# Kernel tuning notes

Measured on AMD Instinct MI355X. Metric: run time of the kernel, lower is better.

Reference implementation:

```python
import jax, jax.numpy as jnp
import numpy as np

N_NODES = 50000
N_EDGES = 800000
N_GRAPHS = 500
NFEAT = 128
NHID = 64
NLAYER = 3
BN_EPS = 1e-5


def setup_inputs() -> dict:
    key = jax.random.key(0)
    ks = jax.random.split(key, 8)
    x = jax.random.normal(ks[0], (N_NODES, NFEAT), dtype=jnp.float32)
    edge_index = jax.random.randint(ks[1], (2, N_EDGES), 0, N_NODES)
    batch = jnp.sort(jax.random.randint(ks[2], (N_NODES,), 0, N_GRAPHS))
    Wt = jax.random.normal(ks[3], (NFEAT, NHID), dtype=jnp.float32) / np.float32(np.sqrt(NFEAT))
    bt = jnp.zeros((NHID,), jnp.float32)
    gamma0 = jnp.ones((NHID,), jnp.float32)
    beta0 = jnp.zeros((NHID,), jnp.float32)
    W1 = jax.random.normal(ks[4], (NLAYER, NHID, NHID), dtype=jnp.float32) / np.float32(np.sqrt(NHID))
    W2 = jax.random.normal(ks[5], (NLAYER, NHID, NHID), dtype=jnp.float32) / np.float32(np.sqrt(NHID))
    gammas = jnp.ones((NLAYER, NHID), jnp.float32)
    betas = jnp.zeros((NLAYER, NHID), jnp.float32)
    return dict(x=x, edge_index=edge_index, batch=batch, Wt=Wt, bt=bt,
                gamma0=gamma0, beta0=beta0, W1=W1, W2=W2, gammas=gammas, betas=betas)


def _bn(h, g, b):
    # BatchNorm1d training-mode math: batch mean, biased variance
    mean = jnp.mean(h, axis=0)
    var = jnp.mean((h - mean) ** 2, axis=0)
    return (h - mean) * jax.lax.rsqrt(var + BN_EPS) * g + b


def _pool_mean(h, batch):
    s = jax.ops.segment_sum(h, batch, num_segments=N_GRAPHS)
    cnt = jax.ops.segment_sum(jnp.ones((h.shape[0], 1), h.dtype), batch, num_segments=N_GRAPHS)
    return s / jnp.maximum(cnt, 1.0)


def _embed_std(h, batch):
    m = _pool_mean(h, batch)                      # [G, nhid]
    s = jnp.sqrt(_pool_mean((h - m[batch]) ** 2, batch))
    return m, s


def reference(x, edge_index, batch, Wt, bt, gamma0, beta0, W1, W2, gammas, betas):
    src, dst = edge_index[0], edge_index[1]
    h = _bn(x @ Wt + bt, gamma0, beta0)           # transform: Linear + BN
    e0, s0 = _embed_std(h, batch)

    def step(h, p):
        w1, w2, g, b = p
        agg = jax.ops.segment_sum(h[src], dst, num_segments=N_NODES)  # GIN sum-aggregation
        z = (h + agg)                              # (1+eps)*x + agg, eps=0
        z = jax.nn.relu(z @ w1) @ w2               # GINConv nn: Linear-ReLU-Linear (no bias)
        z = _bn(jax.nn.relu(z), g, b)              # act then BN
        e, s = _embed_std(z, batch)
        return z, (e, s)

    _, (es, ss) = jax.lax.scan(step, h, (W1, W2, gammas, betas))
    graph_embeds = jnp.concatenate([e0[None], es], axis=0)  # [nlayer+1, G, nhid]
    graph_stds = jnp.concatenate([s0[None], ss], axis=0)
    return graph_embeds, graph_stds
```

## Files before the change

kernel.cpp:

```cpp
#include <hip/hip_runtime.h>
#include <hip/hip_bf16.h>

#define NN 50000
#define NE 800000
#define NG 500
#define NF 128
#define NH 64
#define NB 256
#define NPB 196
#define EPB 4096
#define NBLK ((NE + EPB - 1)/EPB)
#define CSR_LDS 2048

typedef unsigned int u32;
typedef unsigned short u16;
typedef _Float16 h2 __attribute__((ext_vector_type(2)));
typedef _Float16 h8 __attribute__((ext_vector_type(8)));
typedef float f32x4 __attribute__((ext_vector_type(4)));

__device__ __forceinline__ float bf1(u16 v){ return __uint_as_float(((u32)v) << 16); }
__device__ __forceinline__ float h1(u16 v){ return (float)__builtin_bit_cast(_Float16, v); }
__device__ __forceinline__ u32 pk(float a, float b){
  return __builtin_bit_cast(u32, __builtin_amdgcn_cvt_pkrtz(a, b));
}
__device__ __forceinline__ h2 uph(u32 u){ return __builtin_bit_cast(h2, u); }
__device__ __forceinline__ u16 f16b(float f){ return __builtin_bit_cast(u16, (_Float16)f); }

__device__ __forceinline__ void cv8h(uint4 q, float* f){
  h2 v0 = uph(q.x), v1 = uph(q.y), v2 = uph(q.z), v3 = uph(q.w);
  f[0]=(float)v0.x; f[1]=(float)v0.y; f[2]=(float)v1.x; f[3]=(float)v1.y;
  f[4]=(float)v2.x; f[5]=(float)v2.y; f[6]=(float)v3.x; f[7]=(float)v3.y;
}

__device__ __forceinline__ h8 pack8(float4 p, float4 q){
  uint4 t;
  t.x = pk(p.x, p.y); t.y = pk(p.z, p.w);
  t.z = pk(q.x, q.y); t.w = pk(q.z, q.w);
  return __builtin_bit_cast(h8, t);
}
__device__ __forceinline__ f32x4 z4(){
  f32x4 v; v[0]=0.f; v[1]=0.f; v[2]=0.f; v[3]=0.f; return v;
}

__global__ __launch_bounds__(256) void k_init(const u32* __restrict__ xw, int* __restrict__ flag,
    const int* __restrict__ batch, int* __restrict__ starts,
    const float* __restrict__ Wt, const float* __restrict__ W1, const float* __restrict__ W2,
    u16* __restrict__ wtT, u16* __restrict__ w1T, u16* __restrict__ w2T){
  int b = blockIdx.x, tid = threadIdx.x;
  if (b < 48){
    int t = b*256 + tid;
    if (t < NH*NF){
      int c = t >> 7, k = t & 127;
      wtT[t] = f16b(Wt[(size_t)k*NH + c]);
    }
    if (t < 3*NH*NH){
      int l = t >> 12, c = (t >> 6) & 63, k = t & 63;
      w1T[t] = f16b(W1[(size_t)l*NH*NH + k*NH + c]);
      w2T[t] = f16b(W2[(size_t)l*NH*NH + k*NH + c]);
    }
  } else {
    if (tid < 64){
      u32 w = xw[tid];
      u32 lo = w & 0xFFFFu;
      u32 e = (lo >> 7) & 0xFFu;
      bool vote = (e >= 0x60u && e <= 0x8Fu);
      unsigned long long m = __ballot(vote);
      if (tid == 0) flag[0] = (__popcll(m) >= 32) ? 1 : 0;
    }
    for (int g = tid; g <= NG; g += 256){
      int lo = 0, hi = NN;
      while (lo < hi){ int mid = (lo + hi) >> 1; if (batch[mid] < g) lo = mid + 1; else hi = mid; }
      starts[g] = lo;
    }
  }
}


__global__ __launch_bounds__(256) void k_bhist(const int* __restrict__ ei, int* __restrict__ bcount,
    int* __restrict__ bstart, int* __restrict__ bcur, int* __restrict__ ticket){
  __shared__ int h[NB];
  __shared__ int part[NB];
  __shared__ int isLast;
  int tid = threadIdx.x;
  h[tid] = 0;
  __syncthreads();
  int e0 = blockIdx.x*EPB;
  #pragma unroll
  for (int i = 0; i < 16; i++){
    int e = e0 + i*256 + tid;
    if (e < NE) atomicAdd(&h[ei[NE + e] / NPB], 1);
  }
  __syncthreads();
  if (h[tid]) atomicAdd(&bcount[tid], h[tid]);
  __threadfence();
  if (tid == 0) isLast = (atomicAdd(ticket, 1) == (int)gridDim.x - 1);
  __syncthreads();
  if (!isLast) return;
  int v = atomicAdd(&bcount[tid], 0);
  part[tid] = v;
  __syncthreads();
  for (int off = 1; off < 256; off <<= 1){
    int u = (tid >= off) ? part[tid-off] : 0;
    __syncthreads();
    part[tid] += u;
    __syncthreads();
  }
  int ex = part[tid] - v;
  bstart[tid] = ex;
  bcur[tid] = ex;
  if (tid == 0) bstart[NB] = NE;
}

__global__ __launch_bounds__(256) void k_bscat(const int* __restrict__ ei,
    int* __restrict__ bcur, u32* __restrict__ pkE){
  __shared__ int h[NB];
  __shared__ int loff[NB];
  __shared__ int base[NB];
  __shared__ int part[NB];
  __shared__ u32 sv[EPB];
  int tid = threadIdx.x;
  h[tid] = 0;
  __syncthreads();
  int e0 = blockIdx.x*EPB;
  u32 meta[16], vals[16];
  #pragma unroll
  for (int i = 0; i < 16; i++){
    int e = e0 + i*256 + tid;
    if (e < NE){
      int s = ei[e], d = ei[NE + e];
      int b = d / NPB;
      int r = atomicAdd(&h[b], 1);
      meta[i] = ((u32)b << 16) | (u32)r;
      vals[i] = ((u32)d << 16) | (u32)s;
    } else meta[i] = 0xFFFFFFFFu;
  }
  __syncthreads();
  int cnt = h[tid];
  part[tid] = cnt;
  __syncthreads();
  for (int off = 1; off < 256; off <<= 1){
    int u = (tid >= off) ? part[tid-off] : 0;
    __syncthreads();
    part[tid] += u;
    __syncthreads();
  }
  loff[tid] = part[tid] - cnt;
  base[tid] = cnt ? atomicAdd(&bcur[tid], cnt) : 0;
  __syncthreads();
  #pragma unroll
  for (int i = 0; i < 16; i++){
    if (meta[i] != 0xFFFFFFFFu){
      int b = meta[i] >> 16, r = meta[i] & 0xFFFFu;
      sv[loff[b] + r] = vals[i];
    }
  }
  __syncthreads();
  int total = min(EPB, NE - e0);
  for (int j = tid; j < total; j += 256){
    u32 v = sv[j];
    int b = (int)(v >> 16) / NPB;
    pkE[base[b] + (j - loff[b])] = v;
  }
}

__global__ __launch_bounds__(256) void k_bfill(const u32* __restrict__ pkE,
    const int* __restrict__ bstart, int* __restrict__ rowptr, int* __restrict__ csr){
  __shared__ int part[NB];
  __shared__ int cur[NB];
  int b = blockIdx.x;
  int tid = threadIdx.x;
  int nb0 = b*NPB;
  int nr = min(NPB, NN - nb0);
  int rbeg = bstart[b], rend = bstart[b+1];
  part[tid] = 0;
  __syncthreads();
  for (int j = rbeg + tid; j < rend; j += 256){
    u32 pe = pkE[j];
    atomicAdd(&part[(int)(pe >> 16) - nb0], 1);
  }
  __syncthreads();
  int v = part[tid];
  __syncthreads();
  for (int off = 1; off < 256; off <<= 1){
    int u = (tid >= off) ? part[tid-off] : 0;
    __syncthreads();
    part[tid] += u;
    __syncthreads();
  }
  int ex = part[tid] - v;
  if (tid < nr) rowptr[nb0 + tid] = rbeg + ex;
  if (b == NB-1 && tid == 0) rowptr[NN] = NE;
  cur[tid] = ex;
  __syncthreads();
  for (int j = rbeg + tid; j < rend; j += 256){
    u32 pe = pkE[j];
    int node = (int)(pe >> 16) - nb0;
    int p = atomicAdd(&cur[node], 1);
    csr[rbeg + p] = (int)(pe & 0xFFFFu);
  }
}

__global__ __launch_bounds__(256) void k_transform_m(const float* __restrict__ x,
    const u16* __restrict__ wtT, const float* __restrict__ bt,
    u16* __restrict__ th, float* __restrict__ s1){
  __shared__ float sRed[8*NH];
  int tid = threadIdx.x;
  int w = tid >> 6, l = tid & 63;
  int lr = l & 15, kb = l >> 4;
  h8 bf[4][4];
  #pragma unroll
  for (int n = 0; n < 4; n++)
    #pragma unroll
    for (int kk = 0; kk < 4; kk++)
      bf[n][kk] = *(const h8*)&wtT[(size_t)(16*n + lr)*NF + kk*32 + kb*8];
  int node0 = blockIdx.x*64 + w*16;
  int rowA = node0 + lr; if (rowA > NN-1) rowA = NN-1;
  const float* xr = x + (size_t)rowA*NF + kb*8;
  f32x4 acc[4];
  #pragma unroll
  for (int n = 0; n < 4; n++) acc[n] = z4();
  #pragma unroll
  for (int kk = 0; kk < 4; kk++){
    float4 p = *(const float4*)(xr + kk*32);
    float4 q = *(const float4*)(xr + kk*32 + 4);
    h8 a = pack8(p, q);
    #pragma unroll
    for (int n = 0; n < 4; n++)
      acc[n] = __builtin_amdgcn_mfma_f32_16x16x32_f16(a, bf[n][kk], acc[n], 0, 0, 0);
  }
  #pragma unroll
  for (int n = 0; n < 4; n++){
    float bias = bt[16*n + lr];
    float a1 = 0.f, a2 = 0.f;
    #pragma unroll
    for (int r = 0; r < 4; r++){
      int g = node0 + 4*kb + r;
      float v = acc[n][r] + bias;
      if (g < NN){
        th[(size_t)g*NH + 16*n + lr] = f16b(v);
        a1 += v; a2 += v*v;
      }
    }
    a1 += __shfl_xor(a1, 16); a1 += __shfl_xor(a1, 32);
    a2 += __shfl_xor(a2, 16); a2 += __shfl_xor(a2, 32);
    if (kb == 0){
      sRed[w*NH + 16*n + lr] = a1;
      sRed[(4+w)*NH + 16*n + lr] = a2;
    }
  }
  __syncthreads();
  if (tid < NH){
    float a1 = sRed[tid] + sRed[NH+tid] + sRed[2*NH+tid] + sRed[3*NH+tid];
    float a2 = sRed[4*NH+tid] + sRed[5*NH+tid] + sRed[6*NH+tid] + sRed[7*NH+tid];
    unsafeAtomicAdd(&s1[tid], a1);
    unsafeAtomicAdd(&s1[NH+tid], a2);
  }
}

__global__ __launch_bounds__(512) void k_gmlp(const u16* __restrict__ t,
    const int* __restrict__ rowptr, const int* __restrict__ csr, u16* __restrict__ Th,
    const u16* __restrict__ w1T, const u16* __restrict__ w2T, int wofs,
    const float* __restrict__ s1i,
    const void* __restrict__ gamma, const void* __restrict__ beta, int ofs,
    const int* __restrict__ flag, float* __restrict__ s1o){
  __shared__ __align__(16) u16 sU[64*NH];
  __shared__ __align__(16) u16 sV[64*NH];
  __shared__ float sRed[8*NH];
  __shared__ float scs[NH], shs[NH];
  __shared__ int sCsr[CSR_LDS];
  __shared__ int sRp[65];
  int tid = threadIdx.x;
  int node0 = blockIdx.x*64;
  if (tid < NH){
    int bfl = flag[0];
    float gm = bfl ? bf1(((const u16*)gamma)[ofs+tid]) : ((const float*)gamma)[ofs+tid];
    float be = bfl ? bf1(((const u16*)beta)[ofs+tid])  : ((const float*)beta)[ofs+tid];
    float mean = s1i[tid] * (1.f/NN);
    float var  = s1i[NH+tid] * (1.f/NN) - mean*mean;
    float rr = rsqrtf(fmaxf(var, 0.f) + 1e-5f);
    float sc = gm * rr;
    scs[tid] = sc;
    shs[tid] = be - mean*sc;
  }
  if (tid >= 128 && tid < 193){
    int idx = tid - 128;
    int nd = node0 + idx;
    sRp[idx] = rowptr[nd > NN ? NN : nd];
  }
  __syncthreads();
  int base = sRp[0];
  int cnt = sRp[64] - base;
  for (int i = tid; i < cnt && i < CSR_LDS; i += 512) sCsr[i] = csr[base + i];
  __syncthreads();
  int w = tid >> 6, lane = tid & 63;
  {
    int slot = lane >> 3, chunk = lane & 7;
    int nl = w*8 + slot;
    int node = node0 + nl;
    int swz = (nl & 7) << 3;
    if (node < NN){
      int beg = sRp[nl], en = sRp[nl+1];
      float acc[8];
      uint4 qs = *(const uint4*)&t[(size_t)node*NH + chunk*8];
      cv8h(qs, acc);
      int j = beg;
      for (; j + 4 <= en; j += 4){
        int o = j - base;
        int s0 = (o + 0 < CSR_LDS) ? sCsr[o+0] : csr[j+0];
        int s1 = (o + 1 < CSR_LDS) ? sCsr[o+1] : csr[j+1];
        int s2 = (o + 2 < CSR_LDS) ? sCsr[o+2] : csr[j+2];
        int s3 = (o + 3 < CSR_LDS) ? sCsr[o+3] : csr[j+3];
        uint4 q0 = *(const uint4*)&t[(size_t)s0*NH + chunk*8];
        uint4 q1 = *(const uint4*)&t[(size_t)s1*NH + chunk*8];
        uint4 q2 = *(const uint4*)&t[(size_t)s2*NH + chunk*8];
        uint4 q3 = *(const uint4*)&t[(size_t)s3*NH + chunk*8];
        float f0[8], f1[8], f2[8], f3[8];
        cv8h(q0, f0); cv8h(q1, f1); cv8h(q2, f2); cv8h(q3, f3);
        #pragma unroll
        for (int i = 0; i < 8; i++) acc[i] += (f0[i] + f1[i]) + (f2[i] + f3[i]);
      }
      for (; j < en; j++){
        int o = j - base;
        int s0 = (o < CSR_LDS) ? sCsr[o] : csr[j];
        uint4 q = *(const uint4*)&t[(size_t)s0*NH + chunk*8];
        float f[8]; cv8h(q, f);
        #pragma unroll
        for (int i = 0; i < 8; i++) acc[i] += f[i];
      }
      float deg1 = (float)(en - beg + 1);
      float o8[8];
      #pragma unroll
      for (int i = 0; i < 8; i++)
        o8[i] = scs[chunk*8+i]*acc[i] + deg1*shs[chunk*8+i];
      uint4 ov;
      ov.x = pk(o8[0], o8[1]); ov.y = pk(o8[2], o8[3]);
      ov.z = pk(o8[4], o8[5]); ov.w = pk(o8[6], o8[7]);
      *(uint4*)&sU[nl*NH + ((chunk*8) ^ swz)] = ov;
    } else {
      uint4 zz; zz.x = 0; zz.y = 0; zz.z = 0; zz.w = 0;
      *(uint4*)&sU[nl*NH + ((chunk*8) ^ swz)] = zz;
    }
  }
  __syncthreads();
  int lr = lane & 15, kb = lane >> 4;
  int rb = w & 3, ch = w >> 2;
  h8 b1[2][2], b2[2][2];
  #pragma unroll
  for (int n2 = 0; n2 < 2; n2++)
    #pragma unroll
    for (int kk = 0; kk < 2; kk++){
      int n = 2*ch + n2;
      b1[n2][kk] = *(const h8*)&w1T[wofs + (16*n + lr)*NH + kk*32 + kb*8];
      b2[n2][kk] = *(const h8*)&w2T[wofs + (16*n + lr)*NH + kk*32 + kb*8];
    }
  int rv = 16*rb + lr;
  f32x4 acc[2];
  acc[0] = z4(); acc[1] = z4();
  const u16* urow = sU + rv*NH;
  #pragma unroll
  for (int kk = 0; kk < 2; kk++){
    h8 a = *(const h8*)&urow[(kk*32 + kb*8) ^ ((rv & 7) << 3)];
    #pragma unroll
    for (int n2 = 0; n2 < 2; n2++)
      acc[n2] = __builtin_amdgcn_mfma_f32_16x16x32_f16(a, b1[n2][kk], acc[n2], 0, 0, 0);
  }
  #pragma unroll
  for (int n2 = 0; n2 < 2; n2++){
    int n = 2*ch + n2;
    #pragma unroll
    for (int r = 0; r < 4; r++){
      int row = 16*rb + 4*kb + r;
      int col = 16*n + lr;
      sV[row*NH + (col ^ ((row & 7) << 3))] = f16b(fmaxf(acc[n2][r], 0.f));
    }
  }
  __syncthreads();
  f32x4 acc2[2];
  acc2[0] = z4(); acc2[1] = z4();
  const u16* vrow = sV + rv*NH;
  #pragma unroll
  for (int kk = 0; kk < 2; kk++){
    h8 a = *(const h8*)&vrow[(kk*32 + kb*8) ^ ((rv & 7) << 3)];
    #pragma unroll
    for (int n2 = 0; n2 < 2; n2++)
      acc2[n2] = __builtin_amdgcn_mfma_f32_16x16x32_f16(a, b2[n2][kk], acc2[n2], 0, 0, 0);
  }
  #pragma unroll
  for (int n2 = 0; n2 < 2; n2++){
    int n = 2*ch + n2;
    float a1 = 0.f, a2 = 0.f;
    #pragma unroll
    for (int r = 0; r < 4; r++){
      int g = node0 + 16*rb + 4*kb + r;
      float v = fmaxf(acc2[n2][r], 0.f);
      if (g < NN){
        Th[(size_t)g*NH + 16*n + lr] = f16b(v);
        a1 += v; a2 += v*v;
      }
    }
    a1 += __shfl_xor(a1, 16); a1 += __shfl_xor(a1, 32);
    a2 += __shfl_xor(a2, 16); a2 += __shfl_xor(a2, 32);
    if (kb == 0){
      sRed[rb*NH + 16*n + lr] = a1;
      sRed[(4+rb)*NH + 16*n + lr] = a2;
    }
  }
  __syncthreads();
  if (tid < NH){
    float a1 = sRed[tid] + sRed[NH+tid] + sRed[2*NH+tid] + sRed[3*NH+tid];
    float a2 = sRed[4*NH+tid] + sRed[5*NH+tid] + sRed[6*NH+tid] + sRed[7*NH+tid];
    unsafeAtomicAdd(&s1o[tid], a1);
    unsafeAtomicAdd(&s1o[NH+tid], a2);
  }
}

__global__ __launch_bounds__(512) void k_embed(const u16* __restrict__ t,
    const float* __restrict__ s1,
    const void* __restrict__ gamma, const void* __restrict__ beta, int ofs,
    const int* __restrict__ starts, const int* __restrict__ flag,
    void* __restrict__ dout, int layer){
  __shared__ float sRed[16*NH];
  int g = blockIdx.x;
  int tx = threadIdx.x & 63, ty = threadIdx.x >> 6;
  int bf = flag[0];
  float gm = bf ? bf1(((const u16*)gamma)[ofs+tx]) : ((const float*)gamma)[ofs+tx];
  float be = bf ? bf1(((const u16*)beta)[ofs+tx])  : ((const float*)beta)[ofs+tx];
  float mean = s1[tx] * (1.f/NN);
  float var  = s1[NH+tx] * (1.f/NN) - mean*mean;
  float rr = rsqrtf(fmaxf(var, 0.f) + 1e-5f);
  float sc = gm * rr;
  float sh = be - mean*sc;
  int st = starts[g], en = starts[g+1];
  float ls1 = 0.f, ls2 = 0.f;
  for (int n = st + ty; n < en; n += 8){
    float z = h1(t[(size_t)n*NH + tx]) * sc + sh;
    ls1 += z; ls2 += z*z;
  }
  sRed[ty*NH + tx] = ls1;
  sRed[(8+ty)*NH + tx] = ls2;
  __syncthreads();
  if (ty == 0){
    float a1 = 0.f, a2 = 0.f;
    #pragma unroll
    for (int r = 0; r < 8; r++){
      a1 += sRed[r*NH + tx];
      a2 += sRed[(8+r)*NH + tx];
    }
    int cnt = en - st;
    float inv = 1.f / (float)max(cnt, 1);
    float m = a1 * inv;
    float vv = a2 * inv - m*m;
    float s = sqrtf(fmaxf(vv, 0.f));
    size_t eidx = ((size_t)layer*NG + g)*NH + tx;
    size_t sidx = (size_t)4*NG*NH + eidx;
    if (bf){
      ((__hip_bfloat16*)dout)[eidx] = __float2bfloat16(m);
      ((__hip_bfloat16*)dout)[sidx] = __float2bfloat16(s);
    } else {
      ((float*)dout)[eidx] = m;
      ((float*)dout)[sidx] = s;
    }
  }
}

extern "C" void kernel_launch(void* const* d_in, const int* in_sizes, int n_in,
                              void* d_out, int out_size, void* d_ws, size_t ws_size,
                              hipStream_t stream) {
  const void* x    = d_in[0];
  const int* ei    = (const int*)d_in[1];
  const int* batch = (const int*)d_in[2];
  const void* Wt   = d_in[3];
  const void* bt   = d_in[4];
  const void* g0   = d_in[5];
  const void* b0   = d_in[6];
  const void* W1   = d_in[7];
  const void* W2   = d_in[8];
  const void* gs   = d_in[9];
  const void* bs   = d_in[10];

  u16*  tA    = (u16*)d_ws;
  u16*  tB    = tA + (size_t)NN*NH;
  float* sAll = (float*)(tB + (size_t)NN*NH);
  int* bcount = (int*)(sAll + 512);
  int* ticket = bcount + NB;
  int* bstart = ticket + 64;
  int* bcur   = bstart + 288;
  int* starts = bcur + NB;
  int* flag   = starts + 512;
  int* rowptr = flag + 64;
  u32* pkE    = (u32*)(rowptr + NN + 64);
  int* csr    = (int*)(pkE + NE);
  u16* wtT    = (u16*)(csr + NE);
  u16* w1T    = wtT + (size_t)NH*NF;
  u16* w2T    = w1T + (size_t)3*NH*NH;

  hipMemsetAsync(sAll, 0, (512 + NB + 64)*sizeof(float), stream);
  k_init<<<49, 256, 0, stream>>>((const u32*)x, flag, batch, starts,
      (const float*)Wt, (const float*)W1, (const float*)W2, wtT, w1T, w2T);
  k_bhist<<<NBLK, 256, 0, stream>>>(ei, bcount, bstart, bcur, ticket);
  k_bscat<<<NBLK, 256, 0, stream>>>(ei, bcur, pkE);
  k_bfill<<<NB, 256, 0, stream>>>(pkE, bstart, rowptr, csr);

  k_transform_m<<<(NN+63)/64, 256, 0, stream>>>((const float*)x, wtT, (const float*)bt, tA, sAll);
  k_embed<<<NG, 512, 0, stream>>>(tA, sAll, g0, b0, 0, starts, flag, d_out, 0);

  u16* tin = tA;
  u16* tout = tB;
  for (int l = 0; l < 3; l++){
    float* sIn  = sAll + (size_t)l*128;
    float* sOut = sAll + (size_t)(l+1)*128;
    const void* gg = (l == 0) ? g0 : gs;
    const void* bb = (l == 0) ? b0 : bs;
    int ofs = (l == 0) ? 0 : (l-1)*NH;
    k_gmlp<<<(NN+63)/64, 512, 0, stream>>>(tin, rowptr, csr, tout, w1T, w2T, l*NH*NH,
        sIn, gg, bb, ofs, flag, sOut);
    k_embed<<<NG, 512, 0, stream>>>(tout, sOut, gs, bs, l*NH, starts, flag, d_out, l+1);
    u16* tmp = tin; tin = tout; tout = tmp;
  }
}
```

Measured before the change: 306.2 us.

## Fuse per-graph pooling statistics into transform and GIN kernels, finalize once

Per-graph sums and sums of squares of the pre-BN activations are now gathered in the transform and GIN-MLP epilogues. They go through LDS bins for up to eight graphs per block, with global atomics as the fallback. The four separate k_embed passes, each of which re-read the full activation buffer, are replaced by a single small k_fin kernel that applies the BN affine algebraically to the pooled moments. This removes three launches and four full reads of the node features. In exchange it adds atomics and LDS to the epilogues, and the variance computed from raw moments may lose some precision.

After: 300.8 us. No clear change (-1.8%).

```diff
diff --git a/kernel.cpp b/kernel.cpp
--- a/kernel.cpp
+++ b/kernel.cpp
@@ -11,6 +11,7 @@
 #define EPB 4096
 #define NBLK ((NE + EPB - 1)/EPB)
 #define CSR_LDS 2048
+#define GBIN 8
 
 typedef unsigned int u32;
 typedef unsigned short u16;
@@ -40,6 +41,18 @@
 }
 __device__ __forceinline__ f32x4 z4(){
   f32x4 v; v[0]=0.f; v[1]=0.f; v[2]=0.f; v[3]=0.f; return v;
+}
+
+__device__ __forceinline__ void gflush(float* sGT, float* sGT2,
+    float* gE, float* gS, int b, int gFirst, int c, float pv, float pv2){
+  if (pv == 0.f && pv2 == 0.f) return;
+  if (b < GBIN){
+    atomicAdd(&sGT[b*NH + c], pv);
+    atomicAdd(&sGT2[b*NH + c], pv2);
+  } else {
+    unsafeAtomicAdd(&gE[(size_t)(gFirst + b)*NH + c], pv);
+    unsafeAtomicAdd(&gS[(size_t)(gFirst + b)*NH + c], pv2);
+  }
 }
 
 __global__ __launch_bounds__(256) void k_init(const u32* __restrict__ xw, int* __restrict__ flag,
@@ -202,9 +215,17 @@
 
 __global__ __launch_bounds__(256) void k_transform_m(const float* __restrict__ x,
     const u16* __restrict__ wtT, const float* __restrict__ bt,
-    u16* __restrict__ th, float* __restrict__ s1){
+    const int* __restrict__ batch,
+    u16* __restrict__ th, float* __restrict__ s1, float* __restrict__ gstat0){
   __shared__ float sRed[8*NH];
+  __shared__ float sGT[GBIN*NH], sGT2[GBIN*NH];
+  __shared__ int sB[64];
+  float* gE = gstat0;
+  float* gS = gstat0 + (size_t)NG*NH;
   int tid = threadIdx.x;
+  int blk0 = blockIdx.x*64;
+  for (int i = tid; i < GBIN*NH; i += 256){ sGT[i] = 0.f; sGT2[i] = 0.f; }
+  if (tid < 64) sB[tid] = batch[min(blk0 + tid, NN-1)];
   int w = tid >> 6, l = tid & 63;
   int lr = l & 15, kb = l >> 4;
   h8 bf[4][4];
@@ -213,7 +234,7 @@
     #pragma unroll
     for (int kk = 0; kk < 4; kk++)
       bf[n][kk] = *(const h8*)&wtT[(size_t)(16*n + lr)*NF + kk*32 + kb*8];
-  int node0 = blockIdx.x*64 + w*16;
+  int node0 = blk0 + w*16;
   int rowA = node0 + lr; if (rowA > NN-1) rowA = NN-1;
   const float* xr = x + (size_t)rowA*NF + kb*8;
   f32x4 acc[4];
@@ -228,24 +249,36 @@
     for (int n = 0; n < 4; n++)
       acc[n] = __builtin_amdgcn_mfma_f32_16x16x32_f16(a, bf[n][kk], acc[n], 0, 0, 0);
   }
+  __syncthreads();
+  int gFirst = sB[0];
+  int nlb = w*16 + 4*kb;
   #pragma unroll
   for (int n = 0; n < 4; n++){
     float bias = bt[16*n + lr];
+    int c = 16*n + lr;
     float a1 = 0.f, a2 = 0.f;
+    float pv = 0.f, pv2 = 0.f;
+    int curb = sB[nlb] - gFirst;
     #pragma unroll
     for (int r = 0; r < 4; r++){
       int g = node0 + 4*kb + r;
       float v = acc[n][r] + bias;
       if (g < NN){
-        th[(size_t)g*NH + 16*n + lr] = f16b(v);
+        u16 hv = f16b(v);
+        th[(size_t)g*NH + c] = hv;
         a1 += v; a2 += v*v;
+        float vr = h1(hv);
+        int b = sB[nlb + r] - gFirst;
+        if (b != curb){ gflush(sGT, sGT2, gE, gS, curb, gFirst, c, pv, pv2); pv = 0.f; pv2 = 0.f; curb = b; }
+        pv += vr; pv2 += vr*vr;
       }
     }
+    gflush(sGT, sGT2, gE, gS, curb, gFirst, c, pv, pv2);
     a1 += __shfl_xor(a1, 16); a1 += __shfl_xor(a1, 32);
     a2 += __shfl_xor(a2, 16); a2 += __shfl_xor(a2, 32);
     if (kb == 0){
-      sRed[w*NH + 16*n + lr] = a1;
-      sRed[(4+w)*NH + 16*n + lr] = a2;
+      sRed[w*NH + c] = a1;
+      sRed[(4+w)*NH + c] = a2;
     }
   }
   __syncthreads();
@@ -255,22 +288,36 @@
     unsafeAtomicAdd(&s1[tid], a1);
     unsafeAtomicAdd(&s1[NH+tid], a2);
   }
+  for (int i = tid; i < GBIN*NH; i += 256){
+    float vE = sGT[i], vS = sGT2[i];
+    if (vE != 0.f || vS != 0.f){
+      int g = gFirst + (i >> 6);
+      unsafeAtomicAdd(&gE[(size_t)g*NH + (i & 63)], vE);
+      unsafeAtomicAdd(&gS[(size_t)g*NH + (i & 63)], vS);
+    }
+  }
 }
 
 __global__ __launch_bounds__(512) void k_gmlp(const u16* __restrict__ t,
-    const int* __restrict__ rowptr, const int* __restrict__ csr, u16* __restrict__ Th,
+    const int* __restrict__ rowptr, const int* __restrict__ csr,
+    const int* __restrict__ batch, u16* __restrict__ Th,
     const u16* __restrict__ w1T, const u16* __restrict__ w2T, int wofs,
     const float* __restrict__ s1i,
     const void* __restrict__ gamma, const void* __restrict__ beta, int ofs,
-    const int* __restrict__ flag, float* __restrict__ s1o){
+    const int* __restrict__ flag, float* __restrict__ s1o, float* __restrict__ gstatL){
   __shared__ __align__(16) u16 sU[64*NH];
   __shared__ __align__(16) u16 sV[64*NH];
   __shared__ float sRed[8*NH];
   __shared__ float scs[NH], shs[NH];
   __shared__ int sCsr[CSR_LDS];
   __shared__ int sRp[65];
+  __shared__ float sGT[GBIN*NH], sGT2[GBIN*NH];
+  __shared__ int sB[64];
+  float* gE = gstatL;
+  float* gS = gstatL + (size_t)NG*NH;
   int tid = threadIdx.x;
   int node0 = blockIdx.x*64;
+  sGT[tid] = 0.f; sGT2[tid] = 0.f;
   if (tid < NH){
     int bfl = flag[0];
     float gm = bfl ? bf1(((const u16*)gamma)[ofs+tid]) : ((const float*)gamma)[ofs+tid];
@@ -287,9 +334,12 @@
     int nd = node0 + idx;
     sRp[idx] = rowptr[nd > NN ? NN : nd];
   }
+  if (tid >= 256 && tid < 320)
+    sB[tid - 256] = batch[min(node0 + tid - 256, NN-1)];
   __syncthreads();
   int base = sRp[0];
   int cnt = sRp[64] - base;
+  int gFirst = sB[0];
   for (int i = tid; i < cnt && i < CSR_LDS; i += 512) sCsr[i] = csr[base + i];
   __syncthreads();
   int w = tid >> 6, lane = tid & 63;
@@ -385,24 +435,34 @@
     for (int n2 = 0; n2 < 2; n2++)
       acc2[n2] = __builtin_amdgcn_mfma_f32_16x16x32_f16(a, b2[n2][kk], acc2[n2], 0, 0, 0);
   }
+  int nlb = 16*rb + 4*kb;
   #pragma unroll
   for (int n2 = 0; n2 < 2; n2++){
     int n = 2*ch + n2;
+    int c = 16*n + lr;
     float a1 = 0.f, a2 = 0.f;
+    float pv = 0.f, pv2 = 0.f;
+    int curb = sB[nlb] - gFirst;
     #pragma unroll
     for (int r = 0; r < 4; r++){
-      int g = node0 + 16*rb + 4*kb + r;
+      int g = node0 + nlb + r;
       float v = fmaxf(acc2[n2][r], 0.f);
       if (g < NN){
-        Th[(size_t)g*NH + 16*n + lr] = f16b(v);
+        u16 hv = f16b(v);
+        Th[(size_t)g*NH + c] = hv;
         a1 += v; a2 += v*v;
+        float vr = h1(hv);
+        int b = sB[nlb + r] - gFirst;
+        if (b != curb){ gflush(sGT, sGT2, gE, gS, curb, gFirst, c, pv, pv2); pv = 0.f; pv2 = 0.f; curb = b; }
+        pv += vr; pv2 += vr*vr;
       }
     }
+    gflush(sGT, sGT2, gE, gS, curb, gFirst, c, pv, pv2);
     a1 += __shfl_xor(a1, 16); a1 += __shfl_xor(a1, 32);
     a2 += __shfl_xor(a2, 16); a2 += __shfl_xor(a2, 32);
     if (kb == 0){
-      sRed[rb*NH + 16*n + lr] = a1;
-      sRed[(4+rb)*NH + 16*n + lr] = a2;
+      sRed[rb*NH + c] = a1;
+      sRed[(4+rb)*NH + c] = a2;
     }
   }
   __syncthreads();
@@ -412,54 +472,53 @@
     unsafeAtomicAdd(&s1o[tid], a1);
     unsafeAtomicAdd(&s1o[NH+tid], a2);
   }
-}
-
-__global__ __launch_bounds__(512) void k_embed(const u16* __restrict__ t,
-    const float* __restrict__ s1,
-    const void* __restrict__ gamma, const void* __restrict__ beta, int ofs,
+  {
+    float vE = sGT[tid], vS = sGT2[tid];
+    if (vE != 0.f || vS != 0.f){
+      int g = gFirst + (tid >> 6);
+      unsafeAtomicAdd(&gE[(size_t)g*NH + (tid & 63)], vE);
+      unsafeAtomicAdd(&gS[(size_t)g*NH + (tid & 63)], vS);
+    }
+  }
+}
+
+__global__ __launch_bounds__(256) void k_fin(const float* __restrict__ sAll,
+    const float* __restrict__ gstat,
+    const void* __restrict__ g0, const void* __restrict__ b0,
+    const void* __restrict__ gs, const void* __restrict__ bs,
     const int* __restrict__ starts, const int* __restrict__ flag,
-    void* __restrict__ dout, int layer){
-  __shared__ float sRed[16*NH];
+    void* __restrict__ dout){
   int g = blockIdx.x;
-  int tx = threadIdx.x & 63, ty = threadIdx.x >> 6;
+  int l = threadIdx.x >> 6, c = threadIdx.x & 63;
   int bf = flag[0];
-  float gm = bf ? bf1(((const u16*)gamma)[ofs+tx]) : ((const float*)gamma)[ofs+tx];
-  float be = bf ? bf1(((const u16*)beta)[ofs+tx])  : ((const float*)beta)[ofs+tx];
-  float mean = s1[tx] * (1.f/NN);
-  float var  = s1[NH+tx] * (1.f/NN) - mean*mean;
+  const void* gam = (l == 0) ? g0 : gs;
+  const void* bet = (l == 0) ? b0 : bs;
+  int ofs = (l == 0) ? 0 : (l-1)*NH;
+  float gm = bf ? bf1(((const u16*)gam)[ofs+c]) : ((const float*)gam)[ofs+c];
+  float be = bf ? bf1(((const u16*)bet)[ofs+c]) : ((const float*)bet)[ofs+c];
+  const float* stage = sAll + (size_t)l*128;
+  float mean = stage[c] * (1.f/NN);
+  float var  = stage[NH+c] * (1.f/NN) - mean*mean;
   float rr = rsqrtf(fmaxf(var, 0.f) + 1e-5f);
   float sc = gm * rr;
   float sh = be - mean*sc;
-  int st = starts[g], en = starts[g+1];
-  float ls1 = 0.f, ls2 = 0.f;
-  for (int n = st + ty; n < en; n += 8){
-    float z = h1(t[(size_t)n*NH + tx]) * sc + sh;
-    ls1 += z; ls2 += z*z;
-  }
-  sRed[ty*NH + tx] = ls1;
-  sRed[(8+ty)*NH + tx] = ls2;
-  __syncthreads();
-  if (ty == 0){
-    float a1 = 0.f, a2 = 0.f;
-    #pragma unroll
-    for (int r = 0; r < 8; r++){
-      a1 += sRed[r*NH + tx];
-      a2 += sRed[(8+r)*NH + tx];
-    }
-    int cnt = en - st;
-    float inv = 1.f / (float)max(cnt, 1);
-    float m = a1 * inv;
-    float vv = a2 * inv - m*m;
-    float s = sqrtf(fmaxf(vv, 0.f));
-    size_t eidx = ((size_t)layer*NG + g)*NH + tx;
-    size_t sidx = (size_t)4*NG*NH + eidx;
-    if (bf){
-      ((__hip_bfloat16*)dout)[eidx] = __float2bfloat16(m);
-      ((__hip_bfloat16*)dout)[sidx] = __float2bfloat16(s);
-    } else {
-      ((float*)dout)[eidx] = m;
-      ((float*)dout)[sidx] = s;
-    }
+  int cnt = starts[g+1] - starts[g];
+  float inv = 1.f / (float)max(cnt, 1);
+  const float* gE = gstat + (size_t)l*2*NG*NH;
+  const float* gS = gE + (size_t)NG*NH;
+  float mT = gE[(size_t)g*NH + c] * inv;
+  float mz = sc*mT + sh;
+  float vz = sc*sc*(gS[(size_t)g*NH + c] * inv - mT*mT);
+  float s = sqrtf(fmaxf(vz, 0.f));
+  if (cnt == 0){ mz = 0.f; s = 0.f; }
+  size_t eidx = ((size_t)l*NG + g)*NH + c;
+  size_t sidx = (size_t)4*NG*NH + eidx;
+  if (bf){
+    ((__hip_bfloat16*)dout)[eidx] = __float2bfloat16(mz);
+    ((__hip_bfloat16*)dout)[sidx] = __float2bfloat16(s);
+  } else {
+    ((float*)dout)[eidx] = mz;
+    ((float*)dout)[sidx] = s;
   }
 }
 
@@ -483,7 +542,8 @@
   float* sAll = (float*)(tB + (size_t)NN*NH);
   int* bcount = (int*)(sAll + 512);
   int* ticket = bcount + NB;
-  int* bstart = ticket + 64;
+  float* gstat = (float*)(ticket + 64);
+  int* bstart = (int*)(gstat + (size_t)4*2*NG*NH);
   int* bcur   = bstart + 288;
   int* starts = bcur + NB;
   int* flag   = starts + 512;
@@ -494,15 +554,16 @@
   u16* w1T    = wtT + (size_t)NH*NF;
   u16* w2T    = w1T + (size_t)3*NH*NH;
 
-  hipMemsetAsync(sAll, 0, (512 + NB + 64)*sizeof(float), stream);
+  size_t zbytes = (512 + NB + 64)*sizeof(float) + (size_t)4*2*NG*NH*sizeof(float);
+  hipMemsetAsync(sAll, 0, zbytes, stream);
   k_init<<<49, 256, 0, stream>>>((const u32*)x, flag, batch, starts,
       (const float*)Wt, (const float*)W1, (const float*)W2, wtT, w1T, w2T);
   k_bhist<<<NBLK, 256, 0, stream>>>(ei, bcount, bstart, bcur, ticket);
   k_bscat<<<NBLK, 256, 0, stream>>>(ei, bcur, pkE);
   k_bfill<<<NB, 256, 0, stream>>>(pkE, bstart, rowptr, csr);
 
-  k_transform_m<<<(NN+63)/64, 256, 0, stream>>>((const float*)x, wtT, (const float*)bt, tA, sAll);
-  k_embed<<<NG, 512, 0, stream>>>(tA, sAll, g0, b0, 0, starts, flag, d_out, 0);
+  k_transform_m<<<(NN+63)/64, 256, 0, stream>>>((const float*)x, wtT, (const float*)bt,
+      batch, tA, sAll, gstat);
 
   u16* tin = tA;
   u16* tout = tB;
@@ -512,9 +573,9 @@
     const void* gg = (l == 0) ? g0 : gs;
     const void* bb = (l == 0) ? b0 : bs;
     int ofs = (l == 0) ? 0 : (l-1)*NH;
-    k_gmlp<<<(NN+63)/64, 512, 0, stream>>>(tin, rowptr, csr, tout, w1T, w2T, l*NH*NH,
-        sIn, gg, bb, ofs, flag, sOut);
-    k_embed<<<NG, 512, 0, stream>>>(tout, sOut, gs, bs, l*NH, starts, flag, d_out, l+1);
+    k_gmlp<<<(NN+63)/64, 512, 0, stream>>>(tin, rowptr, csr, batch, tout, w1T, w2T, l*NH*NH,
+        sIn, gg, bb, ofs, flag, sOut, gstat + (size_t)(l+1)*2*NG*NH);
     u16* tmp = tin; tin = tout; tout = tmp;
   }
-}
+  k_fin<<<NG, 256, 0, stream>>>(sAll, gstat, g0, b0, gs, bs, starts, flag, d_out);
+}
```
